# Kernel optimization log

Measured on AMD Instinct MI355X. Metric: run time of the kernel, lower is better.

Reference implementation:

```python
import jax, jax.numpy as jnp
import numpy as np

B, T, D = 4, 4096, 1024


def setup_inputs() -> dict:
    key = jax.random.key(0)
    ks = jax.random.split(key, 7)
    s_in = 1.0 / np.sqrt(D)
    return {
        "x": jax.random.normal(ks[0], (B, T, D), dtype=jnp.float32),
        "W_in": jax.random.uniform(ks[1], (D, 2 * D), jnp.float32, -s_in, s_in),
        "b_in": jax.random.uniform(ks[2], (2 * D,), jnp.float32, -s_in, s_in),
        "A": jax.random.normal(ks[3], (D,), dtype=jnp.float32),
        "C": jax.random.normal(ks[4], (D,), dtype=jnp.float32),
        "W_out": jax.random.uniform(ks[5], (D, D), jnp.float32, -s_in, s_in),
        "b_out": jax.random.uniform(ks[6], (D,), jnp.float32, -s_in, s_in),
    }


def _ssm(v, A, C):
    # diagonal linear recurrence: h_t = sigmoid(A) * h_{t-1} + v_t ; y_t = C * h_t
    decay = jax.nn.sigmoid(A)  # (D,)
    vT = jnp.swapaxes(v, 0, 1)  # (T, B, D)

    def step(h, vt):
        h = decay * h + vt
        return h, h

    h0 = jnp.zeros(vT.shape[1:], dtype=v.dtype)
    _, hs = jax.lax.scan(step, h0, vT)  # (T, B, D)
    return jnp.swapaxes(hs, 0, 1) * C  # (B, T, D)


def reference(x, W_in, b_in, A, C, W_out, b_out):
    proj = x @ W_in + b_in  # (B, T, 2D)
    v, gate = jnp.split(proj, 2, axis=-1)
    gate = jax.nn.sigmoid(gate)
    y = gate * _ssm(v, A, C)
    return y @ W_out + b_out
```

## Files before the change

kernel.cpp:

```cpp
#include <hip/hip_runtime.h>
#include <math.h>

#define BDIM 4
#define TDIM 4096
#define DDIM 1024
#define MDIM (BDIM * TDIM)

#define NC  64
#define LCH 64
static_assert(NC * LCH == TDIM, "chunking");

typedef __attribute__((ext_vector_type(8))) short short8;
typedef __attribute__((ext_vector_type(4))) float f32x4;

__device__ __forceinline__ unsigned short f2bf(float f) {
  unsigned int u = __float_as_uint(f);
  unsigned int r = (u + 0x7fffu + ((u >> 16) & 1u)) >> 16;
  return (unsigned short)r;
}
__device__ __forceinline__ float bf2f(unsigned short h) {
  return __uint_as_float(((unsigned int)h) << 16);
}
__device__ __forceinline__ float sigmoidf_(float x) {
  return 1.0f / (1.0f + expf(-x));
}

__global__ __launch_bounds__(256) void prep_x_kernel(const float* __restrict__ x,
                                                     unsigned short* __restrict__ xh,
                                                     int n4) {
  int i = blockIdx.x * 256 + threadIdx.x;
  if (i >= n4) return;
  float4 f = ((const float4*)x)[i];
  ushort4 h;
  h.x = f2bf(f.x);
  h.y = f2bf(f.y);
  h.z = f2bf(f.z);
  h.w = f2bf(f.w);
  ((ushort4*)xh)[i] = h;
}

__global__ __launch_bounds__(256) void wprep_kernel(const float* __restrict__ in,
                                                    unsigned short* __restrict__ oh,
                                                    int K, int N) {
  __shared__ float t[64][65];
  int n0 = blockIdx.x * 64;
  int k0 = blockIdx.y * 64;
#pragma unroll
  for (int i = 0; i < 16; ++i) {
    int idx = i * 256 + threadIdx.x;
    int r = idx >> 6, c = idx & 63;
    t[r][c] = in[(size_t)(k0 + r) * N + (n0 + c)];
  }
  __syncthreads();
#pragma unroll
  for (int i = 0; i < 16; ++i) {
    int idx = i * 256 + threadIdx.x;
    int rn = idx >> 6, ck = idx & 63;
    oh[(size_t)(n0 + rn) * K + (k0 + ck)] = f2bf(t[ck][rn]);
  }
}


#define BARRIER()                                  \
  do {                                             \
    asm volatile("" ::: "memory");                 \
    __builtin_amdgcn_s_barrier();                  \
    asm volatile("" ::: "memory");                 \
  } while (0)

#define RD_A(SET, BK)                                                           \
  _Pragma("unroll") for (int m = 0; m < 4; ++m)                                 \
      SET[m] = *(const short8*)(ldsb + (((BK) ? baseA1 : baseA0) + m * 2048));

#define RD_B(SET, BK)                                                           \
  _Pragma("unroll") for (int n = 0; n < 4; ++n)                                 \
      SET[n] = *(const short8*)(ldsb + 16384 + (((BK) ? baseB1 : baseB0) +      \
                                                n * 2048));

#define MFMA16(ASET, BSET)                                                      \
  _Pragma("unroll") for (int m = 0; m < 4; ++m)                                 \
      _Pragma("unroll") for (int n = 0; n < 4; ++n)                             \
          acc[m][n] = __builtin_amdgcn_mfma_f32_16x16x32_bf16(                  \
              ASET[m], BSET[n], acc[m][n], 0, 0, 0);

#define STAGE(PTR, S, BUFB, KOFF)                                               \
  __builtin_amdgcn_global_load_lds(                                             \
      (const __attribute__((address_space(1))) unsigned int*)((PTR) + off##S +  \
                                                              (KOFF)),          \
      (__attribute__((address_space(3))) unsigned int*)((char*)lds + (BUFB) +   \
                                                        (S) * 4096 +            \
                                                        wave * 1024),           \
      16, 0, 0);

template <int EPI>
__global__ __launch_bounds__(256, 4) void gemm128(const unsigned short* __restrict__ A,
                                                  const unsigned short* __restrict__ B,
                                                  const float* __restrict__ bias,
                                                  float* __restrict__ outF,
                                                  unsigned short* __restrict__ outV,
                                                  unsigned short* __restrict__ outG,
                                                  int nNt, int K) {
  __shared__ unsigned short lds[16384];

  int cpx = gridDim.x >> 3;
  int bid = blockIdx.x;
  int swz = (bid & 7) * cpx + (bid >> 3);
  int mtile = swz / nNt, ntile = swz % nNt;

  int tid = threadIdx.x;
  int wave = tid >> 6, lane = tid & 63;
  int wm = wave >> 1, wn = wave & 1;
  int rA = wm * 64 + (lane & 15);
  int rB = wn * 64 + (lane & 15);
  int kq2 = (lane >> 4) * 16;

  int baseA0 = ((rA << 7) + kq2) ^ ((rA & 7) << 4);
  int baseA1 = ((rA << 7) + kq2 + 64) ^ ((rA & 7) << 4);
  int baseB0 = ((rB << 7) + kq2) ^ ((rB & 7) << 4);
  int baseB1 = ((rB << 7) + kq2 + 64) ^ ((rB & 7) << 4);
  const char* ldsb = (const char*)lds;

#define MKOFF(S) \
  ({ int Lt = (S) * 4096 + tid * 16; int P = Lt ^ (((Lt >> 7) & 7) << 4); \
     ((P >> 7) * (K << 1)) + (P & 127); })
  int off0 = MKOFF(0), off1 = MKOFF(1), off2 = MKOFF(2), off3 = MKOFF(3);
#undef MKOFF

  const char* AgB = (const char*)(A + (size_t)(mtile * 128) * K);
  const char* BgB = (const char*)(B + (size_t)(ntile * 128) * K);

  f32x4 acc[4][4] = {};
  short8 af[4], bf[4];

  int NT = K >> 6;
  for (int t = 0; t < NT; ++t) {
    int k0 = t << 7;
    STAGE(AgB, 0, 0, k0) STAGE(AgB, 1, 0, k0)
    STAGE(AgB, 2, 0, k0) STAGE(AgB, 3, 0, k0)
    STAGE(BgB, 0, 16384, k0) STAGE(BgB, 1, 16384, k0)
    STAGE(BgB, 2, 16384, k0) STAGE(BgB, 3, 16384, k0)
    asm volatile("s_waitcnt vmcnt(0)" ::: "memory");
    BARRIER();
    RD_A(af, 0);
    RD_B(bf, 0);
    MFMA16(af, bf);
    RD_A(af, 1);
    RD_B(bf, 1);
    MFMA16(af, bf);
    BARRIER();
  }

  int row0 = mtile * 128 + wm * 64 + ((lane >> 4) << 2);
  int col0 = ntile * 128 + wn * 64 + (lane & 15);
#pragma unroll
  for (int m = 0; m < 4; ++m) {
#pragma unroll
    for (int n = 0; n < 4; ++n) {
      int col = col0 + n * 16;
      float bv = bias[col];
#pragma unroll
      for (int j = 0; j < 4; ++j) {
        int row = row0 + m * 16 + j;
        float val = acc[m][n][j] + bv;
        if (EPI == 0) {
          outF[(size_t)row * (nNt * 128) + col] = val;
        } else {
          if (col < DDIM)
            outV[(size_t)row * DDIM + col] = f2bf(val);
          else
            outG[(size_t)row * DDIM + (col - DDIM)] = f2bf(sigmoidf_(val));
        }
      }
    }
  }
}

__global__ __launch_bounds__(256) void ssm_phase1(const unsigned short* __restrict__ v,
                                                  const float* __restrict__ A,
                                                  float* __restrict__ chunkh) {
  int b = blockIdx.y, c = blockIdx.x;
  int d0 = threadIdx.x * 4;
  float4 a4 = *(const float4*)&A[d0];
  float dx = sigmoidf_(a4.x), dy = sigmoidf_(a4.y), dz = sigmoidf_(a4.z), dw = sigmoidf_(a4.w);
  float hx = 0.f, hy = 0.f, hz = 0.f, hw = 0.f;
  const ushort4* vp = (const ushort4*)(v + ((size_t)b * TDIM + (size_t)c * LCH) * DDIM + d0);
#pragma unroll 4
  for (int i = 0; i < LCH; ++i) {
    ushort4 vv = vp[(size_t)i * (DDIM / 4)];
    hx = fmaf(dx, hx, bf2f(vv.x));
    hy = fmaf(dy, hy, bf2f(vv.y));
    hz = fmaf(dz, hz, bf2f(vv.z));
    hw = fmaf(dw, hw, bf2f(vv.w));
  }
  float4 o = {hx, hy, hz, hw};
  *(float4*)&chunkh[(size_t)(b * NC + c) * DDIM + d0] = o;
}

__global__ __launch_bounds__(256) void ssm_phase2(const float* __restrict__ A,
                                                  float* __restrict__ chunkh) {
  int idx = blockIdx.x * 256 + threadIdx.x;
  int b = idx >> 10, d = idx & 1023;
  float dec = sigmoidf_(A[d]);
  float dL = dec;
#pragma unroll
  for (int i = 0; i < 6; ++i) dL *= dL;
  float hv[NC];
#pragma unroll
  for (int c = 0; c < NC; ++c) hv[c] = chunkh[(size_t)(b * NC + c) * DDIM + d];
  float carry = 0.f;
#pragma unroll
  for (int c = 0; c < NC; ++c) {
    float local = hv[c];
    hv[c] = carry;
    carry = fmaf(dL, carry, local);
  }
#pragma unroll
  for (int c = 0; c < NC; ++c) chunkh[(size_t)(b * NC + c) * DDIM + d] = hv[c];
}

__global__ __launch_bounds__(256) void ssm_phase3(const unsigned short* __restrict__ v,
                                                  const unsigned short* __restrict__ g,
                                                  const float* __restrict__ A,
                                                  const float* __restrict__ C,
                                                  const float* __restrict__ chunkh,
                                                  unsigned short* __restrict__ ybf) {
  int b = blockIdx.y, c = blockIdx.x;
  int d0 = threadIdx.x * 4;
  float4 a4 = *(const float4*)&A[d0];
  float4 c4 = *(const float4*)&C[d0];
  float dx = sigmoidf_(a4.x), dy = sigmoidf_(a4.y), dz = sigmoidf_(a4.z), dw = sigmoidf_(a4.w);
  float4 h0 = *(const float4*)&chunkh[(size_t)(b * NC + c) * DDIM + d0];
  float hx = h0.x, hy = h0.y, hz = h0.z, hw = h0.w;
  size_t base = ((size_t)b * TDIM + (size_t)c * LCH) * DDIM + d0;
  const ushort4* vp = (const ushort4*)(v + base);
  const ushort4* gp = (const ushort4*)(g + base);
  ushort4* yp = (ushort4*)(ybf + base);
#pragma unroll 4
  for (int i = 0; i < LCH; ++i) {
    ushort4 vv = vp[(size_t)i * (DDIM / 4)];
    ushort4 gg = gp[(size_t)i * (DDIM / 4)];
    hx = fmaf(dx, hx, bf2f(vv.x));
    hy = fmaf(dy, hy, bf2f(vv.y));
    hz = fmaf(dz, hz, bf2f(vv.z));
    hw = fmaf(dw, hw, bf2f(vv.w));
    ushort4 yy;
    yy.x = f2bf(bf2f(gg.x) * c4.x * hx);
    yy.y = f2bf(bf2f(gg.y) * c4.y * hy);
    yy.z = f2bf(bf2f(gg.z) * c4.z * hz);
    yy.w = f2bf(bf2f(gg.w) * c4.w * hw);
    yp[(size_t)i * (DDIM / 4)] = yy;
  }
}

extern "C" void kernel_launch(void* const* d_in, const int* in_sizes, int n_in,
                              void* d_out, int out_size, void* d_ws, size_t ws_size,
                              hipStream_t stream) {
  const float* x = (const float*)d_in[0];
  const float* W_in = (const float*)d_in[1];
  const float* b_in = (const float*)d_in[2];
  const float* A = (const float*)d_in[3];
  const float* C = (const float*)d_in[4];
  const float* W_out = (const float*)d_in[5];
  const float* b_out = (const float*)d_in[6];
  float* out = (float*)d_out;

  char* ws = (char*)d_ws;
  const size_t MK = (size_t)MDIM * DDIM;
  unsigned short* xh = (unsigned short*)ws;    ws += MK * 2;
  unsigned short* winh = (unsigned short*)ws;  ws += (size_t)2 * DDIM * DDIM * 2;
  unsigned short* wouth = (unsigned short*)ws; ws += (size_t)DDIM * DDIM * 2;
  unsigned short* v = (unsigned short*)ws;     ws += MK * 2;
  unsigned short* g = (unsigned short*)ws;     ws += MK * 2;
  unsigned short* ybf = (unsigned short*)ws;   ws += MK * 2;
  float* chunkh = (float*)ws;                  ws += (size_t)BDIM * NC * DDIM * 4;

  prep_x_kernel<<<(int)(MK / 4 / 256), 256, 0, stream>>>(x, xh, (int)(MK / 4));
  wprep_kernel<<<dim3(2 * DDIM / 64, DDIM / 64), 256, 0, stream>>>(W_in, winh, DDIM, 2 * DDIM);
  wprep_kernel<<<dim3(DDIM / 64, DDIM / 64), 256, 0, stream>>>(W_out, wouth, DDIM, DDIM);

  gemm128<1><<<(MDIM / 128) * 16, 256, 0, stream>>>(xh, winh, b_in, nullptr, v, g, 16, DDIM);

  ssm_phase1<<<dim3(NC, BDIM), 256, 0, stream>>>(v, A, chunkh);
  ssm_phase2<<<(BDIM * DDIM) / 256, 256, 0, stream>>>(A, chunkh);
  ssm_phase3<<<dim3(NC, BDIM), 256, 0, stream>>>(v, g, A, C, chunkh, ybf);

  gemm128<0><<<(MDIM / 128) * 8, 256, 0, stream>>>(ybf, wouth, b_out, out, nullptr, nullptr,
                                                   8, DDIM);
}
```

Baseline: 179.8 us.

## Fuse SSM chunk-local scan into input GEMM epilogue via weighted reduction

Removes the ssm_phase1 kernel by computing each 64-row chunk's local end state inside the input-projection GEMM epilogue. Each lane forms a decay-power weighted sum (decay^(63-t)) of its bf16-rounded v values, and the sums are reduced across lanes with shuffles. The epilogue is also split into separate branches for the v and gate halves. This saves a kernel launch and a full re-read of v, at the cost of extra exp2/log2 work and registers in the GEMM epilogue, plus a separate chunkp buffer. The power-weighted form may differ slightly numerically from the sequential scan.

```diff
diff --git a/kernel.cpp b/kernel.cpp
--- a/kernel.cpp
+++ b/kernel.cpp
@@ -99,6 +99,8 @@
                                                   float* __restrict__ outF,
                                                   unsigned short* __restrict__ outV,
                                                   unsigned short* __restrict__ outG,
+                                                  const float* __restrict__ Adec,
+                                                  float* __restrict__ chunkp,
                                                   int nNt, int K) {
   __shared__ unsigned short lds[16384];
 
@@ -150,53 +152,76 @@
     BARRIER();
   }
 
-  int row0 = mtile * 128 + wm * 64 + ((lane >> 4) << 2);
+  int q = lane >> 4;
+  int row0 = mtile * 128 + wm * 64 + (q << 2);
   int col0 = ntile * 128 + wn * 64 + (lane & 15);
-#pragma unroll
-  for (int m = 0; m < 4; ++m) {
+
+  if (EPI == 0) {
+#pragma unroll
+    for (int m = 0; m < 4; ++m) {
+#pragma unroll
+      for (int n = 0; n < 4; ++n) {
+        int col = col0 + n * 16;
+        float bv = bias[col];
+#pragma unroll
+        for (int j = 0; j < 4; ++j) {
+          int row = row0 + m * 16 + j;
+          outF[(size_t)row * (nNt * 128) + col] = acc[m][n][j] + bv;
+        }
+      }
+    }
+  } else if (col0 >= DDIM) {
+#pragma unroll
+    for (int m = 0; m < 4; ++m) {
+#pragma unroll
+      for (int n = 0; n < 4; ++n) {
+        int col = col0 + n * 16;
+        float bv = bias[col];
+#pragma unroll
+        for (int j = 0; j < 4; ++j) {
+          int row = row0 + m * 16 + j;
+          outG[(size_t)row * DDIM + (col - DDIM)] = f2bf(sigmoidf_(acc[m][n][j] + bv));
+        }
+      }
+    }
+  } else {
+    float partial[4];
 #pragma unroll
     for (int n = 0; n < 4; ++n) {
       int col = col0 + n * 16;
       float bv = bias[col];
-#pragma unroll
-      for (int j = 0; j < 4; ++j) {
-        int row = row0 + m * 16 + j;
-        float val = acc[m][n][j] + bv;
-        if (EPI == 0) {
-          outF[(size_t)row * (nNt * 128) + col] = val;
-        } else {
-          if (col < DDIM)
-            outV[(size_t)row * DDIM + col] = f2bf(val);
-          else
-            outG[(size_t)row * DDIM + (col - DDIM)] = f2bf(sigmoidf_(val));
+      float dec = sigmoidf_(Adec[col]);
+      float l2d = __log2f(dec);
+      float p = 0.f;
+#pragma unroll
+      for (int m = 0; m < 4; ++m) {
+#pragma unroll
+        for (int j = 0; j < 4; ++j) {
+          int row = row0 + m * 16 + j;
+          unsigned short ush = f2bf(acc[m][n][j] + bv);
+          outV[(size_t)row * DDIM + col] = ush;
+          float w = exp2f((float)(63 - (q * 4 + m * 16 + j)) * l2d);
+          p = fmaf(w, bf2f(ush), p);
         }
       }
-    }
-  }
-}
-
-__global__ __launch_bounds__(256) void ssm_phase1(const unsigned short* __restrict__ v,
-                                                  const float* __restrict__ A,
-                                                  float* __restrict__ chunkh) {
-  int b = blockIdx.y, c = blockIdx.x;
-  int d0 = threadIdx.x * 4;
-  float4 a4 = *(const float4*)&A[d0];
-  float dx = sigmoidf_(a4.x), dy = sigmoidf_(a4.y), dz = sigmoidf_(a4.z), dw = sigmoidf_(a4.w);
-  float hx = 0.f, hy = 0.f, hz = 0.f, hw = 0.f;
-  const ushort4* vp = (const ushort4*)(v + ((size_t)b * TDIM + (size_t)c * LCH) * DDIM + d0);
-#pragma unroll 4
-  for (int i = 0; i < LCH; ++i) {
-    ushort4 vv = vp[(size_t)i * (DDIM / 4)];
-    hx = fmaf(dx, hx, bf2f(vv.x));
-    hy = fmaf(dy, hy, bf2f(vv.y));
-    hz = fmaf(dz, hz, bf2f(vv.z));
-    hw = fmaf(dw, hw, bf2f(vv.w));
-  }
-  float4 o = {hx, hy, hz, hw};
-  *(float4*)&chunkh[(size_t)(b * NC + c) * DDIM + d0] = o;
+      partial[n] = p;
+    }
+#pragma unroll
+    for (int n = 0; n < 4; ++n) {
+      partial[n] += __shfl_xor(partial[n], 16, 64);
+      partial[n] += __shfl_xor(partial[n], 32, 64);
+    }
+    if (q == 0) {
+      int chunkg = mtile * 2 + wm;
+#pragma unroll
+      for (int n = 0; n < 4; ++n)
+        chunkp[(size_t)chunkg * DDIM + col0 + n * 16] = partial[n];
+    }
+  }
 }
 
 __global__ __launch_bounds__(256) void ssm_phase2(const float* __restrict__ A,
+                                                  const float* __restrict__ chunkp,
                                                   float* __restrict__ chunkh) {
   int idx = blockIdx.x * 256 + threadIdx.x;
   int b = idx >> 10, d = idx & 1023;
@@ -206,16 +231,14 @@
   for (int i = 0; i < 6; ++i) dL *= dL;
   float hv[NC];
 #pragma unroll
-  for (int c = 0; c < NC; ++c) hv[c] = chunkh[(size_t)(b * NC + c) * DDIM + d];
+  for (int c = 0; c < NC; ++c) hv[c] = chunkp[(size_t)(b * NC + c) * DDIM + d];
   float carry = 0.f;
 #pragma unroll
   for (int c = 0; c < NC; ++c) {
     float local = hv[c];
-    hv[c] = carry;
+    chunkh[(size_t)(b * NC + c) * DDIM + d] = carry;
     carry = fmaf(dL, carry, local);
   }
-#pragma unroll
-  for (int c = 0; c < NC; ++c) chunkh[(size_t)(b * NC + c) * DDIM + d] = hv[c];
 }
 
 __global__ __launch_bounds__(256) void ssm_phase3(const unsigned short* __restrict__ v,
@@ -272,18 +295,19 @@
   unsigned short* v = (unsigned short*)ws;     ws += MK * 2;
   unsigned short* g = (unsigned short*)ws;     ws += MK * 2;
   unsigned short* ybf = (unsigned short*)ws;   ws += MK * 2;
+  float* chunkp = (float*)ws;                  ws += (size_t)BDIM * NC * DDIM * 4;
   float* chunkh = (float*)ws;                  ws += (size_t)BDIM * NC * DDIM * 4;
 
   prep_x_kernel<<<(int)(MK / 4 / 256), 256, 0, stream>>>(x, xh, (int)(MK / 4));
   wprep_kernel<<<dim3(2 * DDIM / 64, DDIM / 64), 256, 0, stream>>>(W_in, winh, DDIM, 2 * DDIM);
   wprep_kernel<<<dim3(DDIM / 64, DDIM / 64), 256, 0, stream>>>(W_out, wouth, DDIM, DDIM);
 
-  gemm128<1><<<(MDIM / 128) * 16, 256, 0, stream>>>(xh, winh, b_in, nullptr, v, g, 16, DDIM);
-
-  ssm_phase1<<<dim3(NC, BDIM), 256, 0, stream>>>(v, A, chunkh);
-  ssm_phase2<<<(BDIM * DDIM) / 256, 256, 0, stream>>>(A, chunkh);
+  gemm128<1><<<(MDIM / 128) * 16, 256, 0, stream>>>(xh, winh, b_in, nullptr, v, g,
+                                                    A, chunkp, 16, DDIM);
+
+  ssm_phase2<<<(BDIM * DDIM) / 256, 256, 0, stream>>>(A, chunkp, chunkh);
   ssm_phase3<<<dim3(NC, BDIM), 256, 0, stream>>>(v, g, A, C, chunkh, ybf);
 
   gemm128<0><<<(MDIM / 128) * 8, 256, 0, stream>>>(ybf, wouth, b_out, out, nullptr, nullptr,
-                                                   8, DDIM);
-}
+                                                   nullptr, nullptr, 8, DDIM);
+}
```

New measurement: 168.5 us (median of 2 runs). 6.3% less time.
